# Performance work log

Hardware: AMD Instinct MI355X
Metric: run time of the kernel (lower is better)

## Reference

```python
import jax, jax.numpy as jnp
import numpy as np

MARGIN = 0.0  # init kwarg margin=0
EPS = 1e-12


def setup_inputs() -> dict:
    key = jax.random.key(0)
    k1, k2 = jax.random.split(key)
    features = jax.random.normal(k1, (128, 4, 128), dtype=jnp.float32)  # [B, V, D]
    labels = jax.random.randint(k2, (128,), 0, 32)  # [B], 32 classes
    return {"features": features, "labels": labels}


def _safe_sqrt(x):
    # sqrt with zero gradient at x == 0 (diagonal of the distance matrix)
    pos = x > 0
    return jnp.sqrt(jnp.where(pos, x, 1.0)) * pos


def reference(features, labels):
    B, V, D = features.shape
    N = B * V
    # labels.repeat(V) in torch == tile
    lab = jnp.tile(labels, V)  # [N]
    # torch.cat(torch.unbind(features, dim=1), dim=0): view-major stacking
    emb = jnp.transpose(features, (1, 0, 2)).reshape(N, D)  # [N, D]
    # pytorch-metric-learning LpDistance default: L2-normalize embeddings, p=2
    emb = emb / jnp.maximum(jnp.linalg.norm(emb, axis=1, keepdims=True), EPS)
    sq_norm = jnp.sum(emb * emb, axis=1)  # [N]
    sq_dist = sq_norm[:, None] + sq_norm[None, :] - 2.0 * (emb @ emb.T)
    d = _safe_sqrt(jnp.maximum(sq_dist, 0.0))  # [N, N] pairwise euclidean

    same = lab[:, None] == lab[None, :]  # [N, N]
    eye = jnp.eye(N, dtype=bool)
    pos_mask = same & ~eye          # valid (anchor, positive) pairs
    neg_mask = ~same                # valid (anchor, negative) pairs
    # all triplets (a, p, n): labels[a]==labels[p], a!=p, labels[a]!=labels[n]
    trip_mask = pos_mask[:, :, None] & neg_mask[:, None, :]  # [N, N, N]

    # loss[a,p,n] = relu(d(a,p) - d(a,n) + margin), masked to valid triplets
    loss = jnp.maximum(d[:, :, None] - d[:, None, :] + MARGIN, 0.0) * trip_mask

    # AvgNonZeroReducer (pytorch-metric-learning default): mean over losses > 0
    total = jnp.sum(loss)
    n_nonzero = jnp.sum(loss > 0).astype(loss.dtype)
    return jnp.where(n_nonzero > 0, total / n_nonzero, jnp.zeros((), loss.dtype))
```

## Files before the change

kernel.cpp:

```cpp
#include <hip/hip_runtime.h>
#include <math.h>

#define BB 128
#define VV 4
#define NN 512
#define DD 128
#define NT 256

__global__ __launch_bounds__(NT)
void fused_triplet(const float* __restrict__ feat,
                   const int* __restrict__ labels,
                   float* __restrict__ psum,
                   float* __restrict__ pcnt) {
    __shared__ float s_ss[NN];
    __shared__ float s_dot[NN];
    __shared__ float s_pos[NN];
    __shared__ float s_neg[NN];
    __shared__ int   s_lab[BB];
    __shared__ int   s_np, s_nn;
    __shared__ float s_wsum[NT / 64];
    __shared__ unsigned int s_wcnt[NT / 64];

    const int a    = blockIdx.x;
    const int tid  = threadIdx.x;
    const int wave = tid >> 6;
    const int lane = tid & 63;
    const int grp  = lane >> 3;
    const int l8   = lane & 7;

    if (tid < BB) s_lab[tid] = labels[tid];
    if (tid == 0) { s_np = 0; s_nn = 0; }

    const int ab = a & (BB - 1), av = a >> 7;
    const float4* arow = (const float4*)(feat + (size_t)ab * (VV * DD) + av * DD);
    float4 af0 = arow[l8];
    float4 af1 = arow[l8 + 8];
    float4 af2 = arow[l8 + 16];
    float4 af3 = arow[l8 + 24];

    #pragma unroll 4
    for (int it = 0; it < 16; ++it) {
        const int j  = (wave << 7) + (it << 3) + grp;
        const int jb = j & (BB - 1), jv = j >> 7;
        const float4* jrow = (const float4*)(feat + (size_t)jb * (VV * DD) + jv * DD);
        float4 x0 = jrow[l8];
        float4 x1 = jrow[l8 + 8];
        float4 x2 = jrow[l8 + 16];
        float4 x3 = jrow[l8 + 24];

        float ss = 0.f, dt = 0.f;
        ss = fmaf(x0.x, x0.x, fmaf(x0.y, x0.y, fmaf(x0.z, x0.z, fmaf(x0.w, x0.w, ss))));
        ss = fmaf(x1.x, x1.x, fmaf(x1.y, x1.y, fmaf(x1.z, x1.z, fmaf(x1.w, x1.w, ss))));
        ss = fmaf(x2.x, x2.x, fmaf(x2.y, x2.y, fmaf(x2.z, x2.z, fmaf(x2.w, x2.w, ss))));
        ss = fmaf(x3.x, x3.x, fmaf(x3.y, x3.y, fmaf(x3.z, x3.z, fmaf(x3.w, x3.w, ss))));
        dt = fmaf(x0.x, af0.x, fmaf(x0.y, af0.y, fmaf(x0.z, af0.z, fmaf(x0.w, af0.w, dt))));
        dt = fmaf(x1.x, af1.x, fmaf(x1.y, af1.y, fmaf(x1.z, af1.z, fmaf(x1.w, af1.w, dt))));
        dt = fmaf(x2.x, af2.x, fmaf(x2.y, af2.y, fmaf(x2.z, af2.z, fmaf(x2.w, af2.w, dt))));
        dt = fmaf(x3.x, af3.x, fmaf(x3.y, af3.y, fmaf(x3.z, af3.z, fmaf(x3.w, af3.w, dt))));

        #pragma unroll
        for (int off = 4; off > 0; off >>= 1) {
            ss += __shfl_xor(ss, off);
            dt += __shfl_xor(dt, off);
        }
        if (l8 == 0) { s_ss[j] = ss; s_dot[j] = dt; }
    }
    __syncthreads();

    const float ssa  = s_ss[a];
    const float inva = 1.f / fmaxf(sqrtf(ssa), 1e-12f);
    const float sna  = ssa * inva * inva;
    float dreg[2];
    #pragma unroll
    for (int rnd = 0; rnd < 2; ++rnd) {
        const int j = tid + (rnd << 8);
        float ssj  = s_ss[j];
        float invj = 1.f / fmaxf(sqrtf(ssj), 1e-12f);
        float snj  = ssj * invj * invj;
        float dot  = s_dot[j] * inva * invj;
        float sq   = fmaxf(sna + snj - 2.f * dot, 0.f);
        dreg[rnd]  = (sq > 0.f) ? sqrtf(sq) : 0.f;
    }

    const int la = s_lab[a & (BB - 1)];
    #pragma unroll
    for (int rnd = 0; rnd < 2; ++rnd) {
        const int j = tid + (rnd << 8);
        bool same  = (s_lab[j & (BB - 1)] == la);
        bool ispos = same & (j != a);
        bool isneg = !same;
        unsigned long long mp = __ballot(ispos);
        unsigned long long mn = __ballot(isneg);
        int basep = 0, basen = 0;
        if (lane == 0) {
            basep = atomicAdd(&s_np, (int)__popcll(mp));
            basen = atomicAdd(&s_nn, (int)__popcll(mn));
        }
        basep = __shfl(basep, 0);
        basen = __shfl(basen, 0);
        unsigned long long below = (1ull << lane) - 1ull;
        if (ispos) s_pos[basep + (int)__popcll(mp & below)] = dreg[rnd];
        if (isneg) s_neg[basen + (int)__popcll(mn & below)] = dreg[rnd];
    }
    __syncthreads();

    const int np = s_np, nn = s_nn;
    float lsum = 0.f;
    unsigned int lcnt = 0;
    for (int p = 0; p < np; ++p) {
        float dp = s_pos[p];
        for (int n = tid; n < nn; n += NT) {
            float diff = dp - s_neg[n];
            if (diff > 0.f) { lsum += diff; lcnt++; }
        }
    }

    #pragma unroll
    for (int off = 32; off > 0; off >>= 1) {
        lsum += __shfl_down(lsum, off);
        lcnt += __shfl_down(lcnt, off);
    }
    if (lane == 0) { s_wsum[wave] = lsum; s_wcnt[wave] = lcnt; }
    __syncthreads();
    if (tid == 0) {
        psum[a] = s_wsum[0] + s_wsum[1] + s_wsum[2] + s_wsum[3];
        pcnt[a] = (float)(s_wcnt[0] + s_wcnt[1] + s_wcnt[2] + s_wcnt[3]);
    }
}

__global__ __launch_bounds__(NT)
void reduce_final(const float* __restrict__ psum,
                  const float* __restrict__ pcnt,
                  float* __restrict__ out) {
    int tid = threadIdx.x;
    float s = psum[tid] + psum[tid + NT];
    float c = pcnt[tid] + pcnt[tid + NT];
    #pragma unroll
    for (int off = 32; off > 0; off >>= 1) {
        s += __shfl_down(s, off);
        c += __shfl_down(c, off);
    }
    __shared__ float ws[NT / 64], wc[NT / 64];
    if ((tid & 63) == 0) { ws[tid >> 6] = s; wc[tid >> 6] = c; }
    __syncthreads();
    if (tid == 0) {
        float S = ws[0] + ws[1] + ws[2] + ws[3];
        float C = wc[0] + wc[1] + wc[2] + wc[3];
        out[0] = (C > 0.f) ? S / C : 0.f;
    }
}

extern "C" void kernel_launch(void* const* d_in, const int* in_sizes, int n_in,
                              void* d_out, int out_size, void* d_ws, size_t ws_size,
                              hipStream_t stream) {
    const float* feat   = (const float*)d_in[0];
    const int*   labels = (const int*)d_in[1];
    float* out = (float*)d_out;

    float* psum = (float*)d_ws;
    float* pcnt = psum + NN;

    fused_triplet<<<NN, NT, 0, stream>>>(feat, labels, psum, pcnt);
    reduce_final<<<1, NT, 0, stream>>>(psum, pcnt, out);
}
```

Before: 71.40 us.

## Fuse final reduction via cooperative grid sync and process two anchors per block

Halves the grid so each block handles two anchors, sharing one pass over all feature rows to compute dot products for both anchors and reusing the squared-norm work. The separate reduction kernel is removed and replaced with a cooperative-groups grid sync followed by block 0 doing the final sum. This saves a kernel launch and duplicate global loads, but adds grid-wide sync overhead, cooperative-launch requirements and halves the number of parallel blocks on a large GPU.

```diff
diff --git a/kernel.cpp b/kernel.cpp
--- a/kernel.cpp
+++ b/kernel.cpp
@@ -1,19 +1,24 @@
 #include <hip/hip_runtime.h>
+#include <hip/hip_cooperative_groups.h>
 #include <math.h>
+
+namespace cg = cooperative_groups;
 
 #define BB 128
 #define VV 4
 #define NN 512
 #define DD 128
 #define NT 256
+#define NBLK 256
 
 __global__ __launch_bounds__(NT)
-void fused_triplet(const float* __restrict__ feat,
-                   const int* __restrict__ labels,
-                   float* __restrict__ psum,
-                   float* __restrict__ pcnt) {
+void fused_all(const float* __restrict__ feat,
+               const int* __restrict__ labels,
+               float* __restrict__ psum,
+               float* __restrict__ pcnt,
+               float* __restrict__ out) {
     __shared__ float s_ss[NN];
-    __shared__ float s_dot[NN];
+    __shared__ float s_dot[2][NN];
     __shared__ float s_pos[NN];
     __shared__ float s_neg[NN];
     __shared__ int   s_lab[BB];
@@ -21,7 +26,7 @@
     __shared__ float s_wsum[NT / 64];
     __shared__ unsigned int s_wcnt[NT / 64];
 
-    const int a    = blockIdx.x;
+    const int bid  = blockIdx.x;
     const int tid  = threadIdx.x;
     const int wave = tid >> 6;
     const int lane = tid & 63;
@@ -29,89 +34,90 @@
     const int l8   = lane & 7;
 
     if (tid < BB) s_lab[tid] = labels[tid];
-    if (tid == 0) { s_np = 0; s_nn = 0; }
 
-    const int ab = a & (BB - 1), av = a >> 7;
-    const float4* arow = (const float4*)(feat + (size_t)ab * (VV * DD) + av * DD);
-    float4 af0 = arow[l8];
-    float4 af1 = arow[l8 + 8];
-    float4 af2 = arow[l8 + 16];
-    float4 af3 = arow[l8 + 24];
+    const int a0 = bid, a1 = bid + NBLK;
+    const float4* ar0 = (const float4*)(feat + (size_t)(a0 & (BB - 1)) * (VV * DD) + (a0 >> 7) * DD);
+    const float4* ar1 = (const float4*)(feat + (size_t)(a1 & (BB - 1)) * (VV * DD) + (a1 >> 7) * DD);
+    float4 af[4], bf[4];
+    #pragma unroll
+    for (int k = 0; k < 4; ++k) { af[k] = ar0[l8 + 8 * k]; bf[k] = ar1[l8 + 8 * k]; }
 
     #pragma unroll 4
     for (int it = 0; it < 16; ++it) {
         const int j  = (wave << 7) + (it << 3) + grp;
         const int jb = j & (BB - 1), jv = j >> 7;
-        const float4* jrow = (const float4*)(feat + (size_t)jb * (VV * DD) + jv * DD);
-        float4 x0 = jrow[l8];
-        float4 x1 = jrow[l8 + 8];
-        float4 x2 = jrow[l8 + 16];
-        float4 x3 = jrow[l8 + 24];
-
-        float ss = 0.f, dt = 0.f;
-        ss = fmaf(x0.x, x0.x, fmaf(x0.y, x0.y, fmaf(x0.z, x0.z, fmaf(x0.w, x0.w, ss))));
-        ss = fmaf(x1.x, x1.x, fmaf(x1.y, x1.y, fmaf(x1.z, x1.z, fmaf(x1.w, x1.w, ss))));
-        ss = fmaf(x2.x, x2.x, fmaf(x2.y, x2.y, fmaf(x2.z, x2.z, fmaf(x2.w, x2.w, ss))));
-        ss = fmaf(x3.x, x3.x, fmaf(x3.y, x3.y, fmaf(x3.z, x3.z, fmaf(x3.w, x3.w, ss))));
-        dt = fmaf(x0.x, af0.x, fmaf(x0.y, af0.y, fmaf(x0.z, af0.z, fmaf(x0.w, af0.w, dt))));
-        dt = fmaf(x1.x, af1.x, fmaf(x1.y, af1.y, fmaf(x1.z, af1.z, fmaf(x1.w, af1.w, dt))));
-        dt = fmaf(x2.x, af2.x, fmaf(x2.y, af2.y, fmaf(x2.z, af2.z, fmaf(x2.w, af2.w, dt))));
-        dt = fmaf(x3.x, af3.x, fmaf(x3.y, af3.y, fmaf(x3.z, af3.z, fmaf(x3.w, af3.w, dt))));
-
+        const float4* jr = (const float4*)(feat + (size_t)jb * (VV * DD) + jv * DD);
+        float ss = 0.f, d0 = 0.f, d1 = 0.f;
+        #pragma unroll
+        for (int k = 0; k < 4; ++k) {
+            float4 x = jr[l8 + 8 * k];
+            ss = fmaf(x.x, x.x,     fmaf(x.y, x.y,     fmaf(x.z, x.z,     fmaf(x.w, x.w,     ss))));
+            d0 = fmaf(x.x, af[k].x, fmaf(x.y, af[k].y, fmaf(x.z, af[k].z, fmaf(x.w, af[k].w, d0))));
+            d1 = fmaf(x.x, bf[k].x, fmaf(x.y, bf[k].y, fmaf(x.z, bf[k].z, fmaf(x.w, bf[k].w, d1))));
+        }
         #pragma unroll
         for (int off = 4; off > 0; off >>= 1) {
             ss += __shfl_xor(ss, off);
-            dt += __shfl_xor(dt, off);
+            d0 += __shfl_xor(d0, off);
+            d1 += __shfl_xor(d1, off);
         }
-        if (l8 == 0) { s_ss[j] = ss; s_dot[j] = dt; }
+        if (l8 == 0) { s_ss[j] = ss; s_dot[0][j] = d0; s_dot[1][j] = d1; }
     }
     __syncthreads();
 
-    const float ssa  = s_ss[a];
-    const float inva = 1.f / fmaxf(sqrtf(ssa), 1e-12f);
-    const float sna  = ssa * inva * inva;
-    float dreg[2];
-    #pragma unroll
-    for (int rnd = 0; rnd < 2; ++rnd) {
-        const int j = tid + (rnd << 8);
-        float ssj  = s_ss[j];
-        float invj = 1.f / fmaxf(sqrtf(ssj), 1e-12f);
-        float snj  = ssj * invj * invj;
-        float dot  = s_dot[j] * inva * invj;
-        float sq   = fmaxf(sna + snj - 2.f * dot, 0.f);
-        dreg[rnd]  = (sq > 0.f) ? sqrtf(sq) : 0.f;
-    }
-
-    const int la = s_lab[a & (BB - 1)];
-    #pragma unroll
-    for (int rnd = 0; rnd < 2; ++rnd) {
-        const int j = tid + (rnd << 8);
-        bool same  = (s_lab[j & (BB - 1)] == la);
-        bool ispos = same & (j != a);
-        bool isneg = !same;
-        unsigned long long mp = __ballot(ispos);
-        unsigned long long mn = __ballot(isneg);
-        int basep = 0, basen = 0;
-        if (lane == 0) {
-            basep = atomicAdd(&s_np, (int)__popcll(mp));
-            basen = atomicAdd(&s_nn, (int)__popcll(mn));
-        }
-        basep = __shfl(basep, 0);
-        basen = __shfl(basen, 0);
-        unsigned long long below = (1ull << lane) - 1ull;
-        if (ispos) s_pos[basep + (int)__popcll(mp & below)] = dreg[rnd];
-        if (isneg) s_neg[basen + (int)__popcll(mn & below)] = dreg[rnd];
-    }
-    __syncthreads();
-
-    const int np = s_np, nn = s_nn;
     float lsum = 0.f;
     unsigned int lcnt = 0;
-    for (int p = 0; p < np; ++p) {
-        float dp = s_pos[p];
-        for (int n = tid; n < nn; n += NT) {
-            float diff = dp - s_neg[n];
-            if (diff > 0.f) { lsum += diff; lcnt++; }
+    #pragma unroll
+    for (int h = 0; h < 2; ++h) {
+        if (h) __syncthreads();
+        const int a = bid + (h << 8);
+        if (tid == 0) { s_np = 0; s_nn = 0; }
+
+        const float ssa  = s_ss[a];
+        const float inva = 1.f / fmaxf(sqrtf(ssa), 1e-12f);
+        const float sna  = ssa * inva * inva;
+        float dreg[2];
+        #pragma unroll
+        for (int rnd = 0; rnd < 2; ++rnd) {
+            const int j = tid + (rnd << 8);
+            float ssj  = s_ss[j];
+            float invj = 1.f / fmaxf(sqrtf(ssj), 1e-12f);
+            float snj  = ssj * invj * invj;
+            float dot  = s_dot[h][j] * inva * invj;
+            float sq   = fmaxf(sna + snj - 2.f * dot, 0.f);
+            dreg[rnd]  = (sq > 0.f) ? sqrtf(sq) : 0.f;
+        }
+        __syncthreads();
+
+        const int la = s_lab[a & (BB - 1)];
+        #pragma unroll
+        for (int rnd = 0; rnd < 2; ++rnd) {
+            const int j = tid + (rnd << 8);
+            bool same  = (s_lab[j & (BB - 1)] == la);
+            bool ispos = same & (j != a);
+            bool isneg = !same;
+            unsigned long long mp = __ballot(ispos);
+            unsigned long long mn = __ballot(isneg);
+            int basep = 0, basen = 0;
+            if (lane == 0) {
+                basep = atomicAdd(&s_np, (int)__popcll(mp));
+                basen = atomicAdd(&s_nn, (int)__popcll(mn));
+            }
+            basep = __shfl(basep, 0);
+            basen = __shfl(basen, 0);
+            unsigned long long below = (1ull << lane) - 1ull;
+            if (ispos) s_pos[basep + (int)__popcll(mp & below)] = dreg[rnd];
+            if (isneg) s_neg[basen + (int)__popcll(mn & below)] = dreg[rnd];
+        }
+        __syncthreads();
+
+        const int np = s_np, nneg = s_nn;
+        for (int p = 0; p < np; ++p) {
+            float dp = s_pos[p];
+            for (int n = tid; n < nneg; n += NT) {
+                float diff = dp - s_neg[n];
+                if (diff > 0.f) { lsum += diff; lcnt++; }
+            }
         }
     }
 
@@ -123,30 +129,27 @@
     if (lane == 0) { s_wsum[wave] = lsum; s_wcnt[wave] = lcnt; }
     __syncthreads();
     if (tid == 0) {
-        psum[a] = s_wsum[0] + s_wsum[1] + s_wsum[2] + s_wsum[3];
-        pcnt[a] = (float)(s_wcnt[0] + s_wcnt[1] + s_wcnt[2] + s_wcnt[3]);
+        psum[bid] = s_wsum[0] + s_wsum[1] + s_wsum[2] + s_wsum[3];
+        pcnt[bid] = (float)(s_wcnt[0] + s_wcnt[1] + s_wcnt[2] + s_wcnt[3]);
     }
-}
 
-__global__ __launch_bounds__(NT)
-void reduce_final(const float* __restrict__ psum,
-                  const float* __restrict__ pcnt,
-                  float* __restrict__ out) {
-    int tid = threadIdx.x;
-    float s = psum[tid] + psum[tid + NT];
-    float c = pcnt[tid] + pcnt[tid + NT];
-    #pragma unroll
-    for (int off = 32; off > 0; off >>= 1) {
-        s += __shfl_down(s, off);
-        c += __shfl_down(c, off);
-    }
-    __shared__ float ws[NT / 64], wc[NT / 64];
-    if ((tid & 63) == 0) { ws[tid >> 6] = s; wc[tid >> 6] = c; }
-    __syncthreads();
-    if (tid == 0) {
-        float S = ws[0] + ws[1] + ws[2] + ws[3];
-        float C = wc[0] + wc[1] + wc[2] + wc[3];
-        out[0] = (C > 0.f) ? S / C : 0.f;
+    cg::this_grid().sync();
+
+    if (bid == 0) {
+        float s = psum[tid];
+        float c = pcnt[tid];
+        #pragma unroll
+        for (int off = 32; off > 0; off >>= 1) {
+            s += __shfl_down(s, off);
+            c += __shfl_down(c, off);
+        }
+        if (lane == 0) { s_wsum[wave] = s; s_wcnt[wave] = (unsigned int)c; }
+        __syncthreads();
+        if (tid == 0) {
+            float S = s_wsum[0] + s_wsum[1] + s_wsum[2] + s_wsum[3];
+            float C = (float)(s_wcnt[0] + s_wcnt[1] + s_wcnt[2] + s_wcnt[3]);
+            out[0] = (C > 0.f) ? S / C : 0.f;
+        }
     }
 }
 
@@ -158,8 +161,10 @@
     float* out = (float*)d_out;
 
     float* psum = (float*)d_ws;
-    float* pcnt = psum + NN;
+    float* pcnt = psum + NBLK;
 
-    fused_triplet<<<NN, NT, 0, stream>>>(feat, labels, psum, pcnt);
-    reduce_final<<<1, NT, 0, stream>>>(psum, pcnt, out);
+    void* args[] = { (void*)&feat, (void*)&labels, (void*)&psum,
+                     (void*)&pcnt, (void*)&out };
+    hipLaunchCooperativeKernel((void*)fused_all, dim3(NBLK), dim3(NT),
+                               args, 0, stream);
 }
```

After: 108.2 us. 51.5% more time.
